# Kernel tuning notes

Measured on AMD Instinct MI355X. Metric: run time of the kernel, lower is better.

The kernel has to match this reference:

```python
import jax, jax.numpy as jnp
import numpy as np
import math

HID = 4096
SLOTS = 8
HEADS = 8
BD = 512  # bottleneck_dim
HD = BD // HEADS  # effective head dim = 64
B, S = 4, 4096


def setup_inputs() -> dict:
    key = jax.random.key(0)
    ks = jax.random.split(key, 8)
    std = 1.0 / math.sqrt(HID)
    return {
        "hidden_states": jax.random.normal(ks[0], (B, S, HID), dtype=jnp.float32),
        "attention_mask": jax.random.randint(ks[1], (B, S), 0, 2, dtype=jnp.int32),
        "memory_slots": jax.random.normal(ks[2], (SLOTS, HID), dtype=jnp.float32) * std,
        # torch nn.Linear weights are [out_features, in_features]
        "Wq": jax.random.normal(ks[3], (BD, HID), dtype=jnp.float32) * std,
        "Wk": jax.random.normal(ks[4], (BD, HID), dtype=jnp.float32) * std,
        "Wv": jax.random.normal(ks[5], (BD, HID), dtype=jnp.float32) * std,
        "Wo": jax.random.normal(ks[6], (HID, BD), dtype=jnp.float32) * (1.0 / math.sqrt(BD)),
    }


def reference(hidden_states, attention_mask, memory_slots, Wq, Wk, Wv, Wo):
    # Q from learnable slots (same for every batch element): [slots, BD]
    Q = memory_slots @ Wq.T
    Q = Q.reshape(SLOTS, HEADS, HD)                      # n h d
    # K/V from sequence: [b, s, BD] -> [b, s, h, d]
    K = jnp.einsum('bsi,oi->bso', hidden_states, Wk).reshape(B, S, HEADS, HD)
    V = jnp.einsum('bsi,oi->bso', hidden_states, Wv).reshape(B, S, HEADS, HD)
    # scores: [b, h, n, s]
    scores = jnp.einsum('nhd,bshd->bhns', Q, K) / jnp.sqrt(jnp.array(HD, scores_dtype := jnp.float32))
    mask = attention_mask[:, None, None, :]              # [b,1,1,s]
    scores = jnp.where(mask == 0, jnp.finfo(scores.dtype).min, scores)
    attn = jax.nn.softmax(scores, axis=-1)
    # output: [b, n, h, d] -> [b, n, BD]
    out = jnp.einsum('bhns,bshd->bnhd', attn, V).reshape(B, SLOTS, BD)
    # o_proj back to hidden_size
    return jnp.einsum('bnd,od->bno', out, Wo)            # [b, slots, HID]
```

## Files before the change

### kernel.cpp

```cpp
#include <hip/hip_runtime.h>
#include <math.h>

#define HID   4096
#define SLOTS 8
#define HEADS 8
#define BD    512
#define HD    64
#define BB    4
#define SS    4096
#define R64   64
#define LSTR  72
#define KC    1024
#define NKZ   4

typedef __attribute__((ext_vector_type(8))) short bf16x8;
typedef __attribute__((ext_vector_type(4))) float f32x4;

__device__ __forceinline__ unsigned short f2bf(float x) {
  unsigned int u = __builtin_bit_cast(unsigned int, x);
  return (unsigned short)((u + 0x7fffu + ((u >> 16) & 1u)) >> 16);
}

__global__ void q_kernel(const float* __restrict__ ms, const float* __restrict__ Wq,
                         float* __restrict__ Q) {
  int w = (blockIdx.x * blockDim.x + threadIdx.x) >> 6;
  int lane = threadIdx.x & 63;
  if (w >= SLOTS * BD) return;
  int n = w >> 9, o = w & (BD - 1);
  const float* a = ms + n * HID;
  const float* b = Wq + (size_t)o * HID;
  float acc = 0.f;
  for (int i = lane; i < HID; i += 64) acc = fmaf(a[i], b[i], acc);
  #pragma unroll
  for (int off = 32; off; off >>= 1) acc += __shfl_down(acc, off, 64);
  if (lane == 0) Q[w] = acc;
}

__global__ void qw_kernel(const float* __restrict__ Q, const float* __restrict__ Wk,
                          unsigned short* __restrict__ QW) {
  int idx = blockIdx.x * blockDim.x + threadIdx.x;
  int r = idx >> 12, i = idx & (HID - 1);
  int h = r >> 3, n = r & 7;
  const float* q  = Q + n * BD + h * HD;
  const float* wk = Wk + (size_t)(h * HD) * HID + i;
  float acc = 0.f;
  #pragma unroll 8
  for (int d = 0; d < HD; ++d) acc = fmaf(q[d], wk[(size_t)d * HID], acc);
  QW[idx] = f2bf(acc * 0.125f);
}

__global__ __launch_bounds__(256) void scores_mfma(const float* __restrict__ hs,
                                                   const unsigned short* __restrict__ QW,
                                                   float* __restrict__ sp) {
  __shared__ unsigned short As[64 * LSTR];
  __shared__ unsigned short Bs[64 * LSTR];
  const int stile = blockIdx.x, b = blockIdx.y, kz = blockIdx.z;
  const int tid = threadIdx.x;
  const int wv = tid >> 6, lane = tid & 63;
  const int quad = lane >> 4, l16 = lane & 15;
  const int srow = tid >> 2, kc = (tid & 3) << 4;
  const float* hsp = hs + ((size_t)(b * SS + stile * 64 + srow)) * HID + kz * KC + kc;
  const unsigned short* qwp = QW + (size_t)srow * HID + kz * KC + kc;

  f32x4 acc[4] = {};
  float4 fa0 = *(const float4*)(hsp + 0);
  float4 fa1 = *(const float4*)(hsp + 4);
  float4 fa2 = *(const float4*)(hsp + 8);
  float4 fa3 = *(const float4*)(hsp + 12);
  uint4 qb0 = *(const uint4*)(qwp);
  uint4 qb1 = *(const uint4*)(qwp + 8);

  for (int c = 0; c < 16; ++c) {
    __syncthreads();
    union { unsigned short us[16]; uint4 q[2]; } u;
    float f[16] = {fa0.x, fa0.y, fa0.z, fa0.w, fa1.x, fa1.y, fa1.z, fa1.w,
                   fa2.x, fa2.y, fa2.z, fa2.w, fa3.x, fa3.y, fa3.z, fa3.w};
    #pragma unroll
    for (int j = 0; j < 16; ++j) u.us[j] = f2bf(f[j]);
    *(uint4*)&As[srow * LSTR + kc]     = u.q[0];
    *(uint4*)&As[srow * LSTR + kc + 8] = u.q[1];
    *(uint4*)&Bs[srow * LSTR + kc]     = qb0;
    *(uint4*)&Bs[srow * LSTR + kc + 8] = qb1;
    __syncthreads();
    if (c < 15) {
      const float* p = hsp + (size_t)(c + 1) * 64;
      fa0 = *(const float4*)(p + 0);
      fa1 = *(const float4*)(p + 4);
      fa2 = *(const float4*)(p + 8);
      fa3 = *(const float4*)(p + 12);
      const unsigned short* q = qwp + (size_t)(c + 1) * 64;
      qb0 = *(const uint4*)(q);
      qb1 = *(const uint4*)(q + 8);
    }
    #pragma unroll
    for (int ks = 0; ks < 2; ++ks) {
      bf16x8 bfrag = *(const bf16x8*)&Bs[(wv * 16 + l16) * LSTR + ks * 32 + quad * 8];
      #pragma unroll
      for (int mt = 0; mt < 4; ++mt) {
        bf16x8 afrag = *(const bf16x8*)&As[(mt * 16 + l16) * LSTR + ks * 32 + quad * 8];
        acc[mt] = __builtin_amdgcn_mfma_f32_16x16x32_bf16(afrag, bfrag, acc[mt], 0, 0, 0);
      }
    }
  }
  const int r = wv * 16 + l16;
  #pragma unroll
  for (int mt = 0; mt < 4; ++mt) {
    int s = stile * 64 + mt * 16 + quad * 4;
    float4 v = make_float4(acc[mt][0], acc[mt][1], acc[mt][2], acc[mt][3]);
    *(float4*)(sp + ((size_t)((kz * BB + b) * R64 + r)) * SS + s) = v;
  }
}

__global__ __launch_bounds__(256) void softmax_kernel(const float* __restrict__ sp,
                                                      const int* __restrict__ mask,
                                                      unsigned short* __restrict__ attn) {
  int br = blockIdx.x;
  int b = br >> 6;
  int tid = threadIdx.x;
  const float* p0 = sp + ((size_t)(0 * BB * R64) + br) * SS;
  const float* p1 = sp + ((size_t)(1 * BB * R64) + br) * SS;
  const float* p2 = sp + ((size_t)(2 * BB * R64) + br) * SS;
  const float* p3 = sp + ((size_t)(3 * BB * R64) + br) * SS;
  const int* mrow = mask + b * SS;
  float vals[16];
  float mx = -INFINITY;
  #pragma unroll
  for (int j = 0; j < 16; ++j) {
    int s = tid + j * 256;
    float v = p0[s] + p1[s] + p2[s] + p3[s];
    if (mrow[s] == 0) v = -INFINITY;
    vals[j] = v;
    mx = fmaxf(mx, v);
  }
  __shared__ float redm[4], reds[4];
  #pragma unroll
  for (int off = 32; off; off >>= 1) mx = fmaxf(mx, __shfl_down(mx, off, 64));
  if ((tid & 63) == 0) redm[tid >> 6] = mx;
  __syncthreads();
  mx = fmaxf(fmaxf(redm[0], redm[1]), fmaxf(redm[2], redm[3]));
  float sum = 0.f;
  #pragma unroll
  for (int j = 0; j < 16; ++j) { vals[j] = expf(vals[j] - mx); sum += vals[j]; }
  #pragma unroll
  for (int off = 32; off; off >>= 1) sum += __shfl_down(sum, off, 64);
  if ((tid & 63) == 0) reds[tid >> 6] = sum;
  __syncthreads();
  sum = reds[0] + reds[1] + reds[2] + reds[3];
  float inv = 1.f / sum;
  #pragma unroll
  for (int j = 0; j < 16; ++j)
    attn[(size_t)br * SS + tid + j * 256] = f2bf(vals[j] * inv);
}

__global__ __launch_bounds__(256) void ctx_mfma(const unsigned short* __restrict__ attn,
                                                const float* __restrict__ hs,
                                                float* __restrict__ ctxp) {
  __shared__ unsigned short As[64 * LSTR];
  __shared__ unsigned short Bs[64 * LSTR];
  const int itile = blockIdx.x, b = blockIdx.y, kz = blockIdx.z;
  const int tid = threadIdx.x;
  const int wv = tid >> 6, lane = tid & 63;
  const int quad = lane >> 4, l16 = lane & 15;
  const int arow = tid >> 2, asc = (tid & 3) << 4;
  const unsigned short* ap = attn + ((size_t)(b * R64 + arow)) * SS + kz * KC + asc;
  const int p = tid & 31, g = tid >> 5;
  const float* bp0 = hs + ((size_t)(b * SS + kz * KC + 2 * p)) * HID + itile * 64 + g * 8;
  const float* bp1 = bp0 + HID;

  f32x4 acc[4] = {};
  uint4 aa0 = *(const uint4*)(ap);
  uint4 aa1 = *(const uint4*)(ap + 8);
  float4 hb00 = *(const float4*)(bp0);
  float4 hb01 = *(const float4*)(bp0 + 4);
  float4 hb10 = *(const float4*)(bp1);
  float4 hb11 = *(const float4*)(bp1 + 4);

  for (int c = 0; c < 16; ++c) {
    __syncthreads();
    *(uint4*)&As[arow * LSTR + asc]     = aa0;
    *(uint4*)&As[arow * LSTR + asc + 8] = aa1;
    {
      float lo[8] = {hb00.x, hb00.y, hb00.z, hb00.w, hb01.x, hb01.y, hb01.z, hb01.w};
      float hi[8] = {hb10.x, hb10.y, hb10.z, hb10.w, hb11.x, hb11.y, hb11.z, hb11.w};
      #pragma unroll
      for (int j = 0; j < 8; ++j) {
        unsigned int v = (unsigned int)f2bf(lo[j]) | ((unsigned int)f2bf(hi[j]) << 16);
        ((unsigned int*)Bs)[(g * 8 + j) * (LSTR / 2) + p] = v;
      }
    }
    __syncthreads();
    if (c < 15) {
      const unsigned short* an = ap + (size_t)(c + 1) * 64;
      aa0 = *(const uint4*)(an);
      aa1 = *(const uint4*)(an + 8);
      const float* bn0 = bp0 + (size_t)(c + 1) * 64 * HID;
      const float* bn1 = bn0 + HID;
      hb00 = *(const float4*)(bn0);
      hb01 = *(const float4*)(bn0 + 4);
      hb10 = *(const float4*)(bn1);
      hb11 = *(const float4*)(bn1 + 4);
    }
    #pragma unroll
    for (int ks = 0; ks < 2; ++ks) {
      bf16x8 bfrag = *(const bf16x8*)&Bs[(wv * 16 + l16) * LSTR + ks * 32 + quad * 8];
      #pragma unroll
      for (int mt = 0; mt < 4; ++mt) {
        bf16x8 afrag = *(const bf16x8*)&As[(mt * 16 + l16) * LSTR + ks * 32 + quad * 8];
        acc[mt] = __builtin_amdgcn_mfma_f32_16x16x32_bf16(afrag, bfrag, acc[mt], 0, 0, 0);
      }
    }
  }
  const int i = itile * 64 + wv * 16 + l16;
  #pragma unroll
  for (int mt = 0; mt < 4; ++mt) {
    int r0 = mt * 16 + quad * 4;
    #pragma unroll
    for (int j = 0; j < 4; ++j)
      ctxp[((size_t)((kz * BB + b) * R64 + r0 + j)) * HID + i] = acc[mt][j];
  }
}

__global__ void ctxsum_kernel(const float* __restrict__ ctxp, float* __restrict__ ctxs) {
  int idx = blockIdx.x * blockDim.x + threadIdx.x;
  const size_t n4 = (size_t)BB * R64 * HID / 4;
  if ((size_t)idx >= n4) return;
  const float4* a = (const float4*)ctxp;
  float4 v0 = a[idx];
  float4 v1 = a[idx + n4];
  float4 v2 = a[idx + 2 * n4];
  float4 v3 = a[idx + 3 * n4];
  float4 r = make_float4(v0.x + v1.x + v2.x + v3.x, v0.y + v1.y + v2.y + v3.y,
                         v0.z + v1.z + v2.z + v3.z, v0.w + v1.w + v2.w + v3.w);
  ((float4*)ctxs)[idx] = r;
}

__global__ void out_kernel(const float* __restrict__ ctx, const float* __restrict__ Wv,
                           float* __restrict__ out) {
  int w = (blockIdx.x * blockDim.x + threadIdx.x) >> 6;
  int lane = threadIdx.x & 63;
  if (w >= BB * BD) return;
  int b = w >> 9, hd = w & 511, h = hd >> 6;
  const float* wvp = Wv + (size_t)hd * HID;
  const float* cb  = ctx + ((size_t)b * R64 + h * 8) * HID;
  float acc[8] = {};
  for (int i = lane; i < HID; i += 64) {
    float wv = wvp[i];
    #pragma unroll
    for (int n = 0; n < 8; ++n) acc[n] = fmaf(cb[(size_t)n * HID + i], wv, acc[n]);
  }
  #pragma unroll
  for (int n = 0; n < 8; ++n) {
    float a = acc[n];
    #pragma unroll
    for (int off = 32; off; off >>= 1) a += __shfl_down(a, off, 64);
    if (lane == 0) out[((size_t)(b * SLOTS + n)) * BD + hd] = a;
  }
}

__global__ void final_kernel(const float* __restrict__ out, const float* __restrict__ Wo,
                             float* __restrict__ y) {
  int w = (blockIdx.x * blockDim.x + threadIdx.x) >> 6;
  int lane = threadIdx.x & 63;
  if (w >= HID) return;
  const float* wo = Wo + (size_t)w * BD;
  float wreg[8];
  #pragma unroll
  for (int j = 0; j < 8; ++j) wreg[j] = wo[lane + j * 64];
  for (int bn = 0; bn < BB * SLOTS; ++bn) {
    const float* orow = out + bn * BD;
    float acc = 0.f;
    #pragma unroll
    for (int j = 0; j < 8; ++j) acc = fmaf(orow[lane + j * 64], wreg[j], acc);
    #pragma unroll
    for (int off = 32; off; off >>= 1) acc += __shfl_down(acc, off, 64);
    if (lane == 0) y[(size_t)bn * HID + w] = acc;
  }
}

extern "C" void kernel_launch(void* const* d_in, const int* in_sizes, int n_in,
                              void* d_out, int out_size, void* d_ws, size_t ws_size,
                              hipStream_t stream) {
  const float* hs   = (const float*)d_in[0];
  const int*   mask = (const int*)d_in[1];
  const float* ms   = (const float*)d_in[2];
  const float* Wq   = (const float*)d_in[3];
  const float* Wk   = (const float*)d_in[4];
  const float* Wv   = (const float*)d_in[5];
  const float* Wo   = (const float*)d_in[6];

  char* ws = (char*)d_ws;
  float*          Q    = (float*)ws;          ws += 4096 * 4;
  unsigned short* QW   = (unsigned short*)ws; ws += R64 * HID * 2;
  float*          sp   = (float*)ws;          ws += (size_t)NKZ * BB * R64 * SS * 4;
  unsigned short* attn = (unsigned short*)ws; ws += (size_t)BB * R64 * SS * 2;
  float*          ctxp = (float*)ws;          ws += (size_t)NKZ * BB * R64 * HID * 4;
  float*          ctxs = (float*)ws;          ws += (size_t)BB * R64 * HID * 4;
  float*          out  = (float*)ws;

  q_kernel<<<dim3((SLOTS * BD * 64) / 256), 256, 0, stream>>>(ms, Wq, Q);
  qw_kernel<<<dim3((R64 * HID) / 256), 256, 0, stream>>>(Q, Wk, QW);
  scores_mfma<<<dim3(64, 4, 4), 256, 0, stream>>>(hs, QW, sp);
  softmax_kernel<<<dim3(BB * R64), 256, 0, stream>>>(sp, mask, attn);
  ctx_mfma<<<dim3(64, 4, 4), 256, 0, stream>>>(attn, hs, ctxp);
  ctxsum_kernel<<<dim3((BB * R64 * HID / 4) / 256), 256, 0, stream>>>(ctxp, ctxs);
  out_kernel<<<dim3((BB * BD * 64) / 256), 256, 0, stream>>>(ctxs, Wv, out);
  final_kernel<<<dim3((HID * 64) / 256), 256, 0, stream>>>(out, Wo, (float*)d_out);
}
```

Before: 566.1 us.

## Drop split-K partials; retile scores and ctx GEMMs with direct fragment loads

The scores and ctx GEMMs no longer split K four ways, so the partial-sum buffers and the ctxsum reduction kernel are removed, and softmax reads a single score row. Scores now uses 16-row tiles with MFMA fragments loaded straight from global memory, with no LDS staging. Ctx uses 16-column tiles with a small LDS transpose buffer and a two-stage register prefetch. This cuts partial-result traffic and one launch, but each block now runs a long serial K loop. In scores, each wave reloads and reconverts the same hidden-state fragment, because the LDS sharing across waves is gone.

```diff
diff --git a/kernel.cpp b/kernel.cpp
--- a/kernel.cpp
+++ b/kernel.cpp
@@ -10,8 +10,6 @@
 #define SS    4096
 #define R64   64
 #define LSTR  72
-#define KC    1024
-#define NKZ   4
 
 typedef __attribute__((ext_vector_type(8))) short bf16x8;
 typedef __attribute__((ext_vector_type(4))) float f32x4;
@@ -52,63 +50,27 @@
 __global__ __launch_bounds__(256) void scores_mfma(const float* __restrict__ hs,
                                                    const unsigned short* __restrict__ QW,
                                                    float* __restrict__ sp) {
-  __shared__ unsigned short As[64 * LSTR];
-  __shared__ unsigned short Bs[64 * LSTR];
-  const int stile = blockIdx.x, b = blockIdx.y, kz = blockIdx.z;
+  const int stile = blockIdx.x, b = blockIdx.y;
   const int tid = threadIdx.x;
   const int wv = tid >> 6, lane = tid & 63;
   const int quad = lane >> 4, l16 = lane & 15;
-  const int srow = tid >> 2, kc = (tid & 3) << 4;
-  const float* hsp = hs + ((size_t)(b * SS + stile * 64 + srow)) * HID + kz * KC + kc;
-  const unsigned short* qwp = QW + (size_t)srow * HID + kz * KC + kc;
-
-  f32x4 acc[4] = {};
-  float4 fa0 = *(const float4*)(hsp + 0);
-  float4 fa1 = *(const float4*)(hsp + 4);
-  float4 fa2 = *(const float4*)(hsp + 8);
-  float4 fa3 = *(const float4*)(hsp + 12);
-  uint4 qb0 = *(const uint4*)(qwp);
-  uint4 qb1 = *(const uint4*)(qwp + 8);
-
-  for (int c = 0; c < 16; ++c) {
-    __syncthreads();
-    union { unsigned short us[16]; uint4 q[2]; } u;
-    float f[16] = {fa0.x, fa0.y, fa0.z, fa0.w, fa1.x, fa1.y, fa1.z, fa1.w,
-                   fa2.x, fa2.y, fa2.z, fa2.w, fa3.x, fa3.y, fa3.z, fa3.w};
-    #pragma unroll
-    for (int j = 0; j < 16; ++j) u.us[j] = f2bf(f[j]);
-    *(uint4*)&As[srow * LSTR + kc]     = u.q[0];
-    *(uint4*)&As[srow * LSTR + kc + 8] = u.q[1];
-    *(uint4*)&Bs[srow * LSTR + kc]     = qb0;
-    *(uint4*)&Bs[srow * LSTR + kc + 8] = qb1;
-    __syncthreads();
-    if (c < 15) {
-      const float* p = hsp + (size_t)(c + 1) * 64;
-      fa0 = *(const float4*)(p + 0);
-      fa1 = *(const float4*)(p + 4);
-      fa2 = *(const float4*)(p + 8);
-      fa3 = *(const float4*)(p + 12);
-      const unsigned short* q = qwp + (size_t)(c + 1) * 64;
-      qb0 = *(const uint4*)(q);
-      qb1 = *(const uint4*)(q + 8);
-    }
-    #pragma unroll
-    for (int ks = 0; ks < 2; ++ks) {
-      bf16x8 bfrag = *(const bf16x8*)&Bs[(wv * 16 + l16) * LSTR + ks * 32 + quad * 8];
-      #pragma unroll
-      for (int mt = 0; mt < 4; ++mt) {
-        bf16x8 afrag = *(const bf16x8*)&As[(mt * 16 + l16) * LSTR + ks * 32 + quad * 8];
-        acc[mt] = __builtin_amdgcn_mfma_f32_16x16x32_bf16(afrag, bfrag, acc[mt], 0, 0, 0);
-      }
-    }
-  }
-  const int r = wv * 16 + l16;
-  #pragma unroll
-  for (int mt = 0; mt < 4; ++mt) {
-    int s = stile * 64 + mt * 16 + quad * 4;
-    float4 v = make_float4(acc[mt][0], acc[mt][1], acc[mt][2], acc[mt][3]);
-    *(float4*)(sp + ((size_t)((kz * BB + b) * R64 + r)) * SS + s) = v;
-  }
+  const float* ap = hs + ((size_t)(b * SS + stile * 16 + l16)) * HID + quad * 8;
+  const unsigned short* bp = QW + ((size_t)(wv * 16 + l16)) * HID + quad * 8;
+
+  f32x4 acc = {};
+  #pragma unroll 4
+  for (int c = 0; c < 128; ++c) {
+    float4 a0 = *(const float4*)(ap + (size_t)c * 32);
+    float4 a1 = *(const float4*)(ap + (size_t)c * 32 + 4);
+    bf16x8 bfrag = *(const bf16x8*)(bp + (size_t)c * 32);
+    union { unsigned short us[8]; bf16x8 v; } ua;
+    float f[8] = {a0.x, a0.y, a0.z, a0.w, a1.x, a1.y, a1.z, a1.w};
+    #pragma unroll
+    for (int j = 0; j < 8; ++j) ua.us[j] = f2bf(f[j]);
+    acc = __builtin_amdgcn_mfma_f32_16x16x32_bf16(ua.v, bfrag, acc, 0, 0, 0);
+  }
+  float4 v = make_float4(acc[0], acc[1], acc[2], acc[3]);
+  *(float4*)(sp + ((size_t)(b * R64 + wv * 16 + l16)) * SS + stile * 16 + quad * 4) = v;
 }
 
 __global__ __launch_bounds__(256) void softmax_kernel(const float* __restrict__ sp,
@@ -117,17 +79,14 @@
   int br = blockIdx.x;
   int b = br >> 6;
   int tid = threadIdx.x;
-  const float* p0 = sp + ((size_t)(0 * BB * R64) + br) * SS;
-  const float* p1 = sp + ((size_t)(1 * BB * R64) + br) * SS;
-  const float* p2 = sp + ((size_t)(2 * BB * R64) + br) * SS;
-  const float* p3 = sp + ((size_t)(3 * BB * R64) + br) * SS;
+  const float* row = sp + (size_t)br * SS;
   const int* mrow = mask + b * SS;
   float vals[16];
   float mx = -INFINITY;
   #pragma unroll
   for (int j = 0; j < 16; ++j) {
     int s = tid + j * 256;
-    float v = p0[s] + p1[s] + p2[s] + p3[s];
+    float v = row[s];
     if (mrow[s] == 0) v = -INFINITY;
     vals[j] = v;
     mx = fmaxf(mx, v);
@@ -154,84 +113,66 @@
 
 __global__ __launch_bounds__(256) void ctx_mfma(const unsigned short* __restrict__ attn,
                                                 const float* __restrict__ hs,
-                                                float* __restrict__ ctxp) {
-  __shared__ unsigned short As[64 * LSTR];
-  __shared__ unsigned short Bs[64 * LSTR];
-  const int itile = blockIdx.x, b = blockIdx.y, kz = blockIdx.z;
+                                                float* __restrict__ ctx) {
+  __shared__ unsigned short Bs[16 * LSTR];
+  const int itile = blockIdx.x, b = blockIdx.y;
   const int tid = threadIdx.x;
   const int wv = tid >> 6, lane = tid & 63;
   const int quad = lane >> 4, l16 = lane & 15;
-  const int arow = tid >> 2, asc = (tid & 3) << 4;
-  const unsigned short* ap = attn + ((size_t)(b * R64 + arow)) * SS + kz * KC + asc;
   const int p = tid & 31, g = tid >> 5;
-  const float* bp0 = hs + ((size_t)(b * SS + kz * KC + 2 * p)) * HID + itile * 64 + g * 8;
-  const float* bp1 = bp0 + HID;
-
-  f32x4 acc[4] = {};
-  uint4 aa0 = *(const uint4*)(ap);
-  uint4 aa1 = *(const uint4*)(ap + 8);
-  float4 hb00 = *(const float4*)(bp0);
-  float4 hb01 = *(const float4*)(bp0 + 4);
-  float4 hb10 = *(const float4*)(bp1);
-  float4 hb11 = *(const float4*)(bp1 + 4);
-
-  for (int c = 0; c < 16; ++c) {
-    __syncthreads();
-    *(uint4*)&As[arow * LSTR + asc]     = aa0;
-    *(uint4*)&As[arow * LSTR + asc + 8] = aa1;
+  const float* bbase = hs + ((size_t)(b * SS + 2 * p)) * HID + itile * 16 + 2 * g;
+  const unsigned short* ap = attn + ((size_t)(b * R64 + wv * 16 + l16)) * SS + quad * 8;
+
+  f32x4 acc = {};
+  float2 hA0 = *(const float2*)(bbase);
+  float2 hA1 = *(const float2*)(bbase + HID);
+  float2 hB0 = *(const float2*)(bbase + (size_t)64 * HID);
+  float2 hB1 = *(const float2*)(bbase + (size_t)64 * HID + HID);
+
+  for (int cc = 0; cc < 64; cc += 2) {
+    __syncthreads();
     {
-      float lo[8] = {hb00.x, hb00.y, hb00.z, hb00.w, hb01.x, hb01.y, hb01.z, hb01.w};
-      float hi[8] = {hb10.x, hb10.y, hb10.z, hb10.w, hb11.x, hb11.y, hb11.z, hb11.w};
-      #pragma unroll
-      for (int j = 0; j < 8; ++j) {
-        unsigned int v = (unsigned int)f2bf(lo[j]) | ((unsigned int)f2bf(hi[j]) << 16);
-        ((unsigned int*)Bs)[(g * 8 + j) * (LSTR / 2) + p] = v;
-      }
-    }
-    __syncthreads();
-    if (c < 15) {
-      const unsigned short* an = ap + (size_t)(c + 1) * 64;
-      aa0 = *(const uint4*)(an);
-      aa1 = *(const uint4*)(an + 8);
-      const float* bn0 = bp0 + (size_t)(c + 1) * 64 * HID;
-      const float* bn1 = bn0 + HID;
-      hb00 = *(const float4*)(bn0);
-      hb01 = *(const float4*)(bn0 + 4);
-      hb10 = *(const float4*)(bn1);
-      hb11 = *(const float4*)(bn1 + 4);
+      unsigned int v0 = (unsigned int)f2bf(hA0.x) | ((unsigned int)f2bf(hA1.x) << 16);
+      unsigned int v1 = (unsigned int)f2bf(hA0.y) | ((unsigned int)f2bf(hA1.y) << 16);
+      ((unsigned int*)Bs)[(2 * g) * (LSTR / 2) + p]     = v0;
+      ((unsigned int*)Bs)[(2 * g + 1) * (LSTR / 2) + p] = v1;
+    }
+    __syncthreads();
+    if (cc + 2 < 64) {
+      const float* bn = bbase + (size_t)(cc + 2) * 64 * HID;
+      hA0 = *(const float2*)(bn);
+      hA1 = *(const float2*)(bn + HID);
     }
     #pragma unroll
     for (int ks = 0; ks < 2; ++ks) {
-      bf16x8 bfrag = *(const bf16x8*)&Bs[(wv * 16 + l16) * LSTR + ks * 32 + quad * 8];
-      #pragma unroll
-      for (int mt = 0; mt < 4; ++mt) {
-        bf16x8 afrag = *(const bf16x8*)&As[(mt * 16 + l16) * LSTR + ks * 32 + quad * 8];
-        acc[mt] = __builtin_amdgcn_mfma_f32_16x16x32_bf16(afrag, bfrag, acc[mt], 0, 0, 0);
-      }
-    }
-  }
-  const int i = itile * 64 + wv * 16 + l16;
-  #pragma unroll
-  for (int mt = 0; mt < 4; ++mt) {
-    int r0 = mt * 16 + quad * 4;
-    #pragma unroll
-    for (int j = 0; j < 4; ++j)
-      ctxp[((size_t)((kz * BB + b) * R64 + r0 + j)) * HID + i] = acc[mt][j];
-  }
-}
-
-__global__ void ctxsum_kernel(const float* __restrict__ ctxp, float* __restrict__ ctxs) {
-  int idx = blockIdx.x * blockDim.x + threadIdx.x;
-  const size_t n4 = (size_t)BB * R64 * HID / 4;
-  if ((size_t)idx >= n4) return;
-  const float4* a = (const float4*)ctxp;
-  float4 v0 = a[idx];
-  float4 v1 = a[idx + n4];
-  float4 v2 = a[idx + 2 * n4];
-  float4 v3 = a[idx + 3 * n4];
-  float4 r = make_float4(v0.x + v1.x + v2.x + v3.x, v0.y + v1.y + v2.y + v3.y,
-                         v0.z + v1.z + v2.z + v3.z, v0.w + v1.w + v2.w + v3.w);
-  ((float4*)ctxs)[idx] = r;
+      bf16x8 bfrag = *(const bf16x8*)&Bs[l16 * LSTR + ks * 32 + quad * 8];
+      bf16x8 afrag = *(const bf16x8*)(ap + (size_t)cc * 64 + ks * 32);
+      acc = __builtin_amdgcn_mfma_f32_16x16x32_bf16(afrag, bfrag, acc, 0, 0, 0);
+    }
+    __syncthreads();
+    {
+      unsigned int v0 = (unsigned int)f2bf(hB0.x) | ((unsigned int)f2bf(hB1.x) << 16);
+      unsigned int v1 = (unsigned int)f2bf(hB0.y) | ((unsigned int)f2bf(hB1.y) << 16);
+      ((unsigned int*)Bs)[(2 * g) * (LSTR / 2) + p]     = v0;
+      ((unsigned int*)Bs)[(2 * g + 1) * (LSTR / 2) + p] = v1;
+    }
+    __syncthreads();
+    if (cc + 3 < 64) {
+      const float* bn = bbase + (size_t)(cc + 3) * 64 * HID;
+      hB0 = *(const float2*)(bn);
+      hB1 = *(const float2*)(bn + HID);
+    }
+    #pragma unroll
+    for (int ks = 0; ks < 2; ++ks) {
+      bf16x8 bfrag = *(const bf16x8*)&Bs[l16 * LSTR + ks * 32 + quad * 8];
+      bf16x8 afrag = *(const bf16x8*)(ap + (size_t)(cc + 1) * 64 + ks * 32);
+      acc = __builtin_amdgcn_mfma_f32_16x16x32_bf16(afrag, bfrag, acc, 0, 0, 0);
+    }
+  }
+  const int i = itile * 16 + l16;
+  #pragma unroll
+  for (int j = 0; j < 4; ++j)
+    ctx[((size_t)(b * R64 + wv * 16 + quad * 4 + j)) * HID + i] = acc[j];
 }
 
 __global__ void out_kernel(const float* __restrict__ ctx, const float* __restrict__ Wv,
@@ -291,18 +232,16 @@
   char* ws = (char*)d_ws;
   float*          Q    = (float*)ws;          ws += 4096 * 4;
   unsigned short* QW   = (unsigned short*)ws; ws += R64 * HID * 2;
-  float*          sp   = (float*)ws;          ws += (size_t)NKZ * BB * R64 * SS * 4;
+  float*          sp   = (float*)ws;          ws += (size_t)BB * R64 * SS * 4;
   unsigned short* attn = (unsigned short*)ws; ws += (size_t)BB * R64 * SS * 2;
-  float*          ctxp = (float*)ws;          ws += (size_t)NKZ * BB * R64 * HID * 4;
-  float*          ctxs = (float*)ws;          ws += (size_t)BB * R64 * HID * 4;
+  float*          ctx  = (float*)ws;          ws += (size_t)BB * R64 * HID * 4;
   float*          out  = (float*)ws;
 
   q_kernel<<<dim3((SLOTS * BD * 64) / 256), 256, 0, stream>>>(ms, Wq, Q);
   qw_kernel<<<dim3((R64 * HID) / 256), 256, 0, stream>>>(Q, Wk, QW);
-  scores_mfma<<<dim3(64, 4, 4), 256, 0, stream>>>(hs, QW, sp);
+  scores_mfma<<<dim3(256, 4), 256, 0, stream>>>(hs, QW, sp);
   softmax_kernel<<<dim3(BB * R64), 256, 0, stream>>>(sp, mask, attn);
-  ctx_mfma<<<dim3(64, 4, 4), 256, 0, stream>>>(attn, hs, ctxp);
-  ctxsum_kernel<<<dim3((BB * R64 * HID / 4) / 256), 256, 0, stream>>>(ctxp, ctxs);
-  out_kernel<<<dim3((BB * BD * 64) / 256), 256, 0, stream>>>(ctxs, Wv, out);
+  ctx_mfma<<<dim3(256, 4), 256, 0, stream>>>(attn, hs, ctx);
+  out_kernel<<<dim3((BB * BD * 64) / 256), 256, 0, stream>>>(ctx, Wv, out);
   final_kernel<<<dim3((HID * 64) / 256), 256, 0, stream>>>(out, Wo, (float*)d_out);
 }
```

Measured after the change: 691.6 us. 1.22x slower.

## Pre-convert hidden states to bf16 and double-buffer tiles via direct global-to-LDS loads

Applied to the files above, without the earlier changes.

Adds a pass that converts hidden_states to bf16 once, so the scores and ctx GEMMs read half the bytes and no longer convert fp32 to bf16 inside their loops. The scores kernel and the attn operand of ctx now load tiles straight into LDS with global_load_lds, using a double buffer and an XOR-swizzled layout to avoid bank conflicts. The cost is an extra full read of the fp32 input and a write plus reread of a 128MB bf16 copy.

```diff
diff --git a/kernel.cpp b/kernel.cpp
--- a/kernel.cpp
+++ b/kernel.cpp
@@ -12,6 +12,7 @@
 #define LSTR  72
 #define KC    1024
 #define NKZ   4
+#define NT    16
 
 typedef __attribute__((ext_vector_type(8))) short bf16x8;
 typedef __attribute__((ext_vector_type(4))) float f32x4;
@@ -19,6 +20,27 @@
 __device__ __forceinline__ unsigned short f2bf(float x) {
   unsigned int u = __builtin_bit_cast(unsigned int, x);
   return (unsigned short)((u + 0x7fffu + ((u >> 16) & 1u)) >> 16);
+}
+
+__device__ __forceinline__ void gl16(const void* g, void* l) {
+  __builtin_amdgcn_global_load_lds(
+      (const __attribute__((address_space(1))) unsigned int*)g,
+      (__attribute__((address_space(3))) unsigned int*)l, 16, 0, 0);
+}
+
+__global__ __launch_bounds__(256) void hsb_kernel(const float* __restrict__ hs,
+                                                  unsigned short* __restrict__ hsb) {
+  const size_t total = (size_t)BB * SS * HID / 8;
+  size_t stride = (size_t)gridDim.x * blockDim.x;
+  for (size_t u = (size_t)blockIdx.x * blockDim.x + threadIdx.x; u < total; u += stride) {
+    const float* src = hs + u * 8;
+    float4 a = *(const float4*)src;
+    float4 b = *(const float4*)(src + 4);
+    union { unsigned short us[8]; uint4 q; } o;
+    o.us[0] = f2bf(a.x); o.us[1] = f2bf(a.y); o.us[2] = f2bf(a.z); o.us[3] = f2bf(a.w);
+    o.us[4] = f2bf(b.x); o.us[5] = f2bf(b.y); o.us[6] = f2bf(b.z); o.us[7] = f2bf(b.w);
+    *(uint4*)(hsb + u * 8) = o.q;
+  }
 }
 
 __global__ void q_kernel(const float* __restrict__ ms, const float* __restrict__ Wq,
@@ -49,58 +71,54 @@
   QW[idx] = f2bf(acc * 0.125f);
 }
 
-__global__ __launch_bounds__(256) void scores_mfma(const float* __restrict__ hs,
+__global__ __launch_bounds__(256) void scores_mfma(const unsigned short* __restrict__ hsb,
                                                    const unsigned short* __restrict__ QW,
                                                    float* __restrict__ sp) {
-  __shared__ unsigned short As[64 * LSTR];
-  __shared__ unsigned short Bs[64 * LSTR];
+  __shared__ __align__(16) unsigned short As[2][4096];
+  __shared__ __align__(16) unsigned short Bs[2][4096];
   const int stile = blockIdx.x, b = blockIdx.y, kz = blockIdx.z;
   const int tid = threadIdx.x;
   const int wv = tid >> 6, lane = tid & 63;
   const int quad = lane >> 4, l16 = lane & 15;
-  const int srow = tid >> 2, kc = (tid & 3) << 4;
-  const float* hsp = hs + ((size_t)(b * SS + stile * 64 + srow)) * HID + kz * KC + kc;
-  const unsigned short* qwp = QW + (size_t)srow * HID + kz * KC + kc;
+  const int trow = tid >> 3;
+  const int tslot = (tid & 7) << 4;
+  const int scol = tslot ^ ((trow & 7) << 4);
+  const char* aSrc0 = (const char*)hsb +
+      (((size_t)(b * SS + stile * 64 + trow)) * HID + kz * KC) * 2 + scol;
+  const char* aSrc1 = (const char*)hsb +
+      (((size_t)(b * SS + stile * 64 + 32 + trow)) * HID + kz * KC) * 2 + scol;
+  const char* bSrc0 = (const char*)QW + (((size_t)trow) * HID + kz * KC) * 2 + scol;
+  const char* bSrc1 = (const char*)QW + (((size_t)(32 + trow)) * HID + kz * KC) * 2 + scol;
 
   f32x4 acc[4] = {};
-  float4 fa0 = *(const float4*)(hsp + 0);
-  float4 fa1 = *(const float4*)(hsp + 4);
-  float4 fa2 = *(const float4*)(hsp + 8);
-  float4 fa3 = *(const float4*)(hsp + 12);
-  uint4 qb0 = *(const uint4*)(qwp);
-  uint4 qb1 = *(const uint4*)(qwp + 8);
-
-  for (int c = 0; c < 16; ++c) {
-    __syncthreads();
-    union { unsigned short us[16]; uint4 q[2]; } u;
-    float f[16] = {fa0.x, fa0.y, fa0.z, fa0.w, fa1.x, fa1.y, fa1.z, fa1.w,
-                   fa2.x, fa2.y, fa2.z, fa2.w, fa3.x, fa3.y, fa3.z, fa3.w};
-    #pragma unroll
-    for (int j = 0; j < 16; ++j) u.us[j] = f2bf(f[j]);
-    *(uint4*)&As[srow * LSTR + kc]     = u.q[0];
-    *(uint4*)&As[srow * LSTR + kc + 8] = u.q[1];
-    *(uint4*)&Bs[srow * LSTR + kc]     = qb0;
-    *(uint4*)&Bs[srow * LSTR + kc + 8] = qb1;
-    __syncthreads();
-    if (c < 15) {
-      const float* p = hsp + (size_t)(c + 1) * 64;
-      fa0 = *(const float4*)(p + 0);
-      fa1 = *(const float4*)(p + 4);
-      fa2 = *(const float4*)(p + 8);
-      fa3 = *(const float4*)(p + 12);
-      const unsigned short* q = qwp + (size_t)(c + 1) * 64;
-      qb0 = *(const uint4*)(q);
-      qb1 = *(const uint4*)(q + 8);
+  gl16(aSrc0, &As[0][tid * 8]);
+  gl16(aSrc1, &As[0][2048 + tid * 8]);
+  gl16(bSrc0, &Bs[0][tid * 8]);
+  gl16(bSrc1, &Bs[0][2048 + tid * 8]);
+  __syncthreads();
+
+  const int sw = (l16 & 7) << 4;
+  for (int c = 0; c < NT; ++c) {
+    const int cur = c & 1, nxt = cur ^ 1;
+    if (c < NT - 1) {
+      const size_t off = (size_t)(c + 1) * 128;
+      gl16(aSrc0 + off, &As[nxt][tid * 8]);
+      gl16(aSrc1 + off, &As[nxt][2048 + tid * 8]);
+      gl16(bSrc0 + off, &Bs[nxt][tid * 8]);
+      gl16(bSrc1 + off, &Bs[nxt][2048 + tid * 8]);
     }
+    const char* ab = (const char*)&As[cur][0];
+    const char* bb = (const char*)&Bs[cur][0];
     #pragma unroll
     for (int ks = 0; ks < 2; ++ks) {
-      bf16x8 bfrag = *(const bf16x8*)&Bs[(wv * 16 + l16) * LSTR + ks * 32 + quad * 8];
+      bf16x8 bfrag = *(const bf16x8*)(bb + (wv * 16 + l16) * 128 + ((ks * 64 + quad * 16) ^ sw));
       #pragma unroll
       for (int mt = 0; mt < 4; ++mt) {
-        bf16x8 afrag = *(const bf16x8*)&As[(mt * 16 + l16) * LSTR + ks * 32 + quad * 8];
+        bf16x8 afrag = *(const bf16x8*)(ab + (mt * 16 + l16) * 128 + ((ks * 64 + quad * 16) ^ sw));
         acc[mt] = __builtin_amdgcn_mfma_f32_16x16x32_bf16(afrag, bfrag, acc[mt], 0, 0, 0);
       }
     }
+    __syncthreads();
   }
   const int r = wv * 16 + l16;
   #pragma unroll
@@ -153,62 +171,71 @@
 }
 
 __global__ __launch_bounds__(256) void ctx_mfma(const unsigned short* __restrict__ attn,
-                                                const float* __restrict__ hs,
+                                                const unsigned short* __restrict__ hsb,
                                                 float* __restrict__ ctxp) {
-  __shared__ unsigned short As[64 * LSTR];
-  __shared__ unsigned short Bs[64 * LSTR];
+  __shared__ __align__(16) unsigned short As[2][4096];
+  __shared__ __align__(16) unsigned short Bs[2][64 * LSTR];
   const int itile = blockIdx.x, b = blockIdx.y, kz = blockIdx.z;
   const int tid = threadIdx.x;
   const int wv = tid >> 6, lane = tid & 63;
   const int quad = lane >> 4, l16 = lane & 15;
-  const int arow = tid >> 2, asc = (tid & 3) << 4;
-  const unsigned short* ap = attn + ((size_t)(b * R64 + arow)) * SS + kz * KC + asc;
+  const int trow = tid >> 3;
+  const int tslot = (tid & 7) << 4;
+  const int scol = tslot ^ ((trow & 7) << 4);
+  const char* aSrc0 = (const char*)attn +
+      (((size_t)(b * R64 + trow)) * SS + kz * KC) * 2 + scol;
+  const char* aSrc1 = (const char*)attn +
+      (((size_t)(b * R64 + 32 + trow)) * SS + kz * KC) * 2 + scol;
   const int p = tid & 31, g = tid >> 5;
-  const float* bp0 = hs + ((size_t)(b * SS + kz * KC + 2 * p)) * HID + itile * 64 + g * 8;
-  const float* bp1 = bp0 + HID;
+  const unsigned short* hb = hsb + ((size_t)(b * SS + kz * KC + 2 * p)) * HID + itile * 64 + g * 8;
 
   f32x4 acc[4] = {};
-  uint4 aa0 = *(const uint4*)(ap);
-  uint4 aa1 = *(const uint4*)(ap + 8);
-  float4 hb00 = *(const float4*)(bp0);
-  float4 hb01 = *(const float4*)(bp0 + 4);
-  float4 hb10 = *(const float4*)(bp1);
-  float4 hb11 = *(const float4*)(bp1 + 4);
-
-  for (int c = 0; c < 16; ++c) {
-    __syncthreads();
-    *(uint4*)&As[arow * LSTR + asc]     = aa0;
-    *(uint4*)&As[arow * LSTR + asc + 8] = aa1;
-    {
-      float lo[8] = {hb00.x, hb00.y, hb00.z, hb00.w, hb01.x, hb01.y, hb01.z, hb01.w};
-      float hi[8] = {hb10.x, hb10.y, hb10.z, hb10.w, hb11.x, hb11.y, hb11.z, hb11.w};
+  uint4 h0 = *(const uint4*)(hb);
+  uint4 h1 = *(const uint4*)(hb + HID);
+  gl16(aSrc0, &As[0][tid * 8]);
+  gl16(aSrc1, &As[0][2048 + tid * 8]);
+  {
+    const unsigned short* u0 = (const unsigned short*)&h0;
+    const unsigned short* u1 = (const unsigned short*)&h1;
+    unsigned int* bs32 = (unsigned int*)&Bs[0][0];
+    #pragma unroll
+    for (int j = 0; j < 8; ++j)
+      bs32[(g * 8 + j) * (LSTR / 2) + p] = (unsigned int)u0[j] | ((unsigned int)u1[j] << 16);
+  }
+  h0 = *(const uint4*)(hb + (size_t)64 * HID);
+  h1 = *(const uint4*)(hb + (size_t)65 * HID);
+  __syncthreads();
+
+  const int sw = (l16 & 7) << 4;
+  for (int c = 0; c < NT; ++c) {
+    const int cur = c & 1, nxt = cur ^ 1;
+    if (c < NT - 1) {
+      const size_t off = (size_t)(c + 1) * 128;
+      gl16(aSrc0 + off, &As[nxt][tid * 8]);
+      gl16(aSrc1 + off, &As[nxt][2048 + tid * 8]);
+      const unsigned short* u0 = (const unsigned short*)&h0;
+      const unsigned short* u1 = (const unsigned short*)&h1;
+      unsigned int* bs32 = (unsigned int*)&Bs[nxt][0];
       #pragma unroll
-      for (int j = 0; j < 8; ++j) {
-        unsigned int v = (unsigned int)f2bf(lo[j]) | ((unsigned int)f2bf(hi[j]) << 16);
-        ((unsigned int*)Bs)[(g * 8 + j) * (LSTR / 2) + p] = v;
+      for (int j = 0; j < 8; ++j)
+        bs32[(g * 8 + j) * (LSTR / 2) + p] = (unsigned int)u0[j] | ((unsigned int)u1[j] << 16);
+      if (c < NT - 2) {
+        const unsigned short* hn = hb + (size_t)(c + 2) * 64 * HID;
+        h0 = *(const uint4*)(hn);
+        h1 = *(const uint4*)(hn + HID);
+      }
+    }
+    const char* ab = (const char*)&As[cur][0];
+    #pragma unroll
+    for (int ks = 0; ks < 2; ++ks) {
+      bf16x8 bfrag = *(const bf16x8*)&Bs[cur][(wv * 16 + l16) * LSTR + ks * 32 + quad * 8];
+      #pragma unroll
+      for (int mt = 0; mt < 4; ++mt) {
+        bf16x8 afrag = *(const bf16x8*)(ab + (mt * 16 + l16) * 128 + ((ks * 64 + quad * 16) ^ sw));
+        acc[mt] = __builtin_amdgcn_mfma_f32_16x16x32_bf16(afrag, bfrag, acc[mt], 0, 0, 0);
       }
     }
     __syncthreads();
-    if (c < 15) {
-      const unsigned short* an = ap + (size_t)(c + 1) * 64;
-      aa0 = *(const uint4*)(an);
-      aa1 = *(const uint4*)(an + 8);
-      const float* bn0 = bp0 + (size_t)(c + 1) * 64 * HID;
-      const float* bn1 = bn0 + HID;
-      hb00 = *(const float4*)(bn0);
-      hb01 = *(const float4*)(bn0 + 4);
-      hb10 = *(const float4*)(bn1);
-      hb11 = *(const float4*)(bn1 + 4);
-    }
-    #pragma unroll
-    for (int ks = 0; ks < 2; ++ks) {
-      bf16x8 bfrag = *(const bf16x8*)&Bs[(wv * 16 + l16) * LSTR + ks * 32 + quad * 8];
-      #pragma unroll
-      for (int mt = 0; mt < 4; ++mt) {
-        bf16x8 afrag = *(const bf16x8*)&As[(mt * 16 + l16) * LSTR + ks * 32 + quad * 8];
-        acc[mt] = __builtin_amdgcn_mfma_f32_16x16x32_bf16(afrag, bfrag, acc[mt], 0, 0, 0);
-      }
-    }
   }
   const int i = itile * 64 + wv * 16 + l16;
   #pragma unroll
@@ -291,17 +318,19 @@
   char* ws = (char*)d_ws;
   float*          Q    = (float*)ws;          ws += 4096 * 4;
   unsigned short* QW   = (unsigned short*)ws; ws += R64 * HID * 2;
+  unsigned short* hsb  = (unsigned short*)ws; ws += (size_t)BB * SS * HID * 2;
   float*          sp   = (float*)ws;          ws += (size_t)NKZ * BB * R64 * SS * 4;
   unsigned short* attn = (unsigned short*)ws; ws += (size_t)BB * R64 * SS * 2;
   float*          ctxp = (float*)ws;          ws += (size_t)NKZ * BB * R64 * HID * 4;
   float*          ctxs = (float*)ws;          ws += (size_t)BB * R64 * HID * 4;
   float*          out  = (float*)ws;
 
+  hsb_kernel<<<dim3(2048), 256, 0, stream>>>(hs, hsb);
   q_kernel<<<dim3((SLOTS * BD * 64) / 256), 256, 0, stream>>>(ms, Wq, Q);
   qw_kernel<<<dim3((R64 * HID) / 256), 256, 0, stream>>>(Q, Wk, QW);
-  scores_mfma<<<dim3(64, 4, 4), 256, 0, stream>>>(hs, QW, sp);
+  scores_mfma<<<dim3(64, 4, 4), 256, 0, stream>>>(hsb, QW, sp);
   softmax_kernel<<<dim3(BB * R64), 256, 0, stream>>>(sp, mask, attn);
-  ctx_mfma<<<dim3(64, 4, 4), 256, 0, stream>>>(attn, hs, ctxp);
+  ctx_mfma<<<dim3(64, 4, 4), 256, 0, stream>>>(attn, hsb, ctxp);
   ctxsum_kernel<<<dim3((BB * R64 * HID / 4) / 256), 256, 0, stream>>>(ctxp, ctxs);
   out_kernel<<<dim3((BB * BD * 64) / 256), 256, 0, stream>>>(ctxs, Wv, out);
   final_kernel<<<dim3((HID * 64) / 256), 256, 0, stream>>>(out, Wo, (float*)d_out);
```

Measured after the change: 551.5 us. 2.6% less time.
